# Kernel tuning notes

Hardware: AMD Instinct MI355X
Metric: run time of the kernel (lower is better)

Reference implementation:

```python
import jax, jax.numpy as jnp
import numpy as np

FEAT = 1024
HID = 512
DK = 256
N = 8192
KMAX = 8
K_LIST = (2, 4, 8)


def setup_inputs() -> dict:
    key = jax.random.key(0)
    ks = jax.random.split(key, 10)
    def glorot(k, shape):
        lim = np.sqrt(6.0 / (shape[0] + shape[1]))
        return jax.random.uniform(k, shape, jnp.float32, -lim, lim)
    return {
        "input_tensor": jax.random.normal(ks[0], (N, FEAT), jnp.float32),
        "sp_matrix": jax.random.randint(ks[1], (N, KMAX + 1), 0, N, jnp.int64 if jax.config.jax_enable_x64 else jnp.int32),
        "W1": glorot(ks[2], (FEAT, HID)),
        "b1": jnp.zeros((HID,), jnp.float32),
        "Wq": glorot(ks[3], (HID, DK)),
        "Wk": glorot(ks[4], (HID, DK)),
        "Wv": glorot(ks[5], (HID, DK)),
        "bv": jnp.zeros((DK,), jnp.float32),
        "Wout": glorot(ks[6], (DK, 2)),
        "bout": jnp.zeros((2,), jnp.float32),
    }


def reference(input_tensor, sp_matrix, W1, b1, Wq, Wk, Wv, bv, Wout, bout):
    # fc1: Dense(512, relu)
    dense = jax.nn.relu(input_tensor @ W1 + b1)            # [n, 512]
    # CustomAttention: scaled QK^T over the whole bag
    q = dense @ Wq                                          # [n, 256]
    k = dense @ Wk                                          # [n, 256]
    attn = (q @ k.T) / jnp.sqrt(jnp.float32(DK))            # [n, n]
    value = dense @ Wv + bv                                 # [n, 256]
    pools = []
    for kk in K_LIST:
        idx = sp_matrix[:, : kk + 1]                        # [n, kk+1]
        # sparse adjacency * attention, row-sum == gather attn[i, idx[i,j]] and sum over j
        a_raw = jnp.take_along_axis(attn, idx, axis=1).sum(axis=1)  # [n]
        alpha = jax.nn.softmax(a_raw)                       # [n]
        pools.append(alpha[:, None] * value)                # [n, 256]
    spp = jnp.concatenate(pools, axis=0)                    # [3n, 256]
    # Last_Sigmoid (subtyping=True): sum-pool -> dense -> softmax
    logits = spp.sum(axis=0, keepdims=True) @ Wout + bout   # [1, 2]
    return jax.nn.softmax(logits, axis=-1)
```

## Files before the change

### kernel.cpp

```cpp
#include <hip/hip_runtime.h>
#include <hip/hip_bf16.h>
#include <math.h>

#define FEAT 1024
#define HID  512
#define DK   256
#define NROWS 8192

typedef __attribute__((ext_vector_type(8))) short short8;
typedef __attribute__((ext_vector_type(4))) float floatx4;

__device__ __forceinline__ unsigned short f2bf(float x) {
    union { float f; unsigned u; } u;
    u.f = x;
    unsigned r = u.u;
    r += 0x7fffu + ((r >> 16) & 1u);
    return (unsigned short)(r >> 16);
}
__device__ __forceinline__ float bf2f(unsigned short x) {
    union { unsigned u; float f; } u;
    u.u = ((unsigned)x) << 16;
    return u.f;
}

__device__ __forceinline__ void gld_lds16(const unsigned short* g, unsigned short* l) {
    __builtin_amdgcn_global_load_lds(
        (__attribute__((address_space(1))) void*)(void*)g,
        (__attribute__((address_space(3))) void*)l,
        16, 0, 0);
}

__device__ __forceinline__ short8 cast8(float4 a, float4 b) {
    short8 r;
    r[0] = (short)f2bf(a.x); r[1] = (short)f2bf(a.y);
    r[2] = (short)f2bf(a.z); r[3] = (short)f2bf(a.w);
    r[4] = (short)f2bf(b.x); r[5] = (short)f2bf(b.y);
    r[6] = (short)f2bf(b.z); r[7] = (short)f2bf(b.w);
    return r;
}

__global__ __launch_bounds__(256) void prep_kernel(
    const float* __restrict__ W1, const float* __restrict__ Wq,
    const float* __restrict__ Wk, const float* __restrict__ Wv,
    unsigned short* __restrict__ W1T, unsigned short* __restrict__ WqT,
    unsigned short* __restrict__ WkT, unsigned short* __restrict__ WvT,
    float* __restrict__ P, float* __restrict__ Z, unsigned* __restrict__ counter)
{
    const int b = blockIdx.x;
    const int tid = threadIdx.x;

    if (b == 0) {
        for (int i = tid; i < 3 * DK; i += 256) P[i] = 0.f;
        if (tid < 3) Z[tid] = 0.f;
        if (tid == 0) *counter = 0u;
    }

    int t = b;
    const float* in; unsigned short* outp; int K, N, tn, tk;
    if (t < 512) {
        in = W1; outp = W1T; K = FEAT; N = HID; tn = t & 15; tk = t >> 4;
    } else {
        t -= 512;
        int z = t >> 7, r = t & 127;
        K = HID; N = DK; tn = r & 7; tk = r >> 3;
        in   = (z == 0) ? Wq  : (z == 1) ? Wk  : Wv;
        outp = (z == 0) ? WqT : (z == 1) ? WkT : WvT;
    }
    __shared__ float tt[32][33];
    const int tx = tid & 31, ty = tid >> 5;
    const int n0 = tn * 32, k0 = tk * 32;
    #pragma unroll
    for (int i2 = ty; i2 < 32; i2 += 8)
        tt[i2][tx] = in[(size_t)(k0 + i2) * N + (n0 + tx)];
    __syncthreads();
    #pragma unroll
    for (int i2 = ty; i2 < 32; i2 += 8)
        outp[(size_t)(n0 + i2) * K + (k0 + tx)] = f2bf(tt[tx][i2]);
}

template<int A_F32>
__global__ __launch_bounds__(256) void gemm_mfma(
    const void* __restrict__ Av,
    const unsigned short* __restrict__ BT0, const unsigned short* __restrict__ BT1,
    const unsigned short* __restrict__ BT2,
    const float* __restrict__ bias0, const float* __restrict__ bias1,
    const float* __restrict__ bias2,
    unsigned short* __restrict__ C0, unsigned short* __restrict__ C1,
    unsigned short* __restrict__ C2,
    int N, int K, int relu)
{
    const int z = blockIdx.z;
    const unsigned short* BT = (z == 0) ? BT0 : (z == 1) ? BT1 : BT2;
    const float* bias        = (z == 0) ? bias0 : (z == 1) ? bias1 : bias2;
    unsigned short* C        = (z == 0) ? C0 : (z == 1) ? C1 : C2;

    __shared__ __align__(16) unsigned short As[64 * 64];
    __shared__ __align__(16) unsigned short Bs[128 * 64];

    const int tid  = threadIdx.x;
    const int lane = tid & 63;
    const int wid  = tid >> 6;
    const int wm = wid >> 1, wn = wid & 1;
    const int m0 = blockIdx.x * 64;
    const int n0 = blockIdx.y * 128;

    int arowp[2], asgp[2];
    const float*          ApF[2];
    const unsigned short* ApB[2];
    #pragma unroll
    for (int p = 0; p < 2; ++p) {
        int idx = p * 256 + tid;
        int row = idx >> 3, g = idx & 7;
        int sg = g ^ (row & 7);
        arowp[p] = row; asgp[p] = sg;
        ApF[p] = (const float*)Av + (size_t)(m0 + row) * K + g * 8;
        ApB[p] = (const unsigned short*)Av + (size_t)(m0 + row) * K + sg * 8;
    }
    const unsigned short* Bp[4];
    #pragma unroll
    for (int p = 0; p < 4; ++p) {
        int idx = p * 256 + tid;
        int row = idx >> 3, g = idx & 7;
        int sg = g ^ (row & 7);
        Bp[p] = BT + (size_t)(n0 + row) * K + sg * 8;
    }

    char* AsB = (char*)As;
    char* BsB = (char*)Bs;

    const int gr = lane >> 4;
    int aoff[2][2], boff[2][4];
    #pragma unroll
    for (int ks = 0; ks < 2; ++ks) {
        int gk = ks * 4 + gr;
        #pragma unroll
        for (int i = 0; i < 2; ++i) {
            int ra = wm * 32 + i * 16 + (lane & 15);
            aoff[ks][i] = ra * 128 + ((gk ^ (ra & 7)) * 16);
        }
        #pragma unroll
        for (int jj = 0; jj < 4; ++jj) {
            int rb = wn * 64 + jj * 16 + (lane & 15);
            boff[ks][jj] = rb * 128 + ((gk ^ (rb & 7)) * 16);
        }
    }

    floatx4 acc[2][4];
    #pragma unroll
    for (int i = 0; i < 2; ++i)
        #pragma unroll
        for (int jj = 0; jj < 4; ++jj)
            acc[i][jj] = (floatx4){0.f, 0.f, 0.f, 0.f};

    for (int kt = 0; kt < K; kt += 64) {
        if (A_F32) {
            float4 a00 = *(const float4*)(ApF[0] + kt);
            float4 a01 = *(const float4*)(ApF[0] + kt + 4);
            float4 a10 = *(const float4*)(ApF[1] + kt);
            float4 a11 = *(const float4*)(ApF[1] + kt + 4);
            #pragma unroll
            for (int p = 0; p < 4; ++p)
                gld_lds16(Bp[p] + kt, (unsigned short*)(BsB + p * 4096 + wid * 1024));
            *(short8*)(AsB + arowp[0] * 128 + asgp[0] * 16) = cast8(a00, a01);
            *(short8*)(AsB + arowp[1] * 128 + asgp[1] * 16) = cast8(a10, a11);
        } else {
            #pragma unroll
            for (int p = 0; p < 2; ++p)
                gld_lds16(ApB[p] + kt, (unsigned short*)(AsB + p * 4096 + wid * 1024));
            #pragma unroll
            for (int p = 0; p < 4; ++p)
                gld_lds16(Bp[p] + kt, (unsigned short*)(BsB + p * 4096 + wid * 1024));
        }
        __syncthreads();

        #pragma unroll
        for (int ks = 0; ks < 2; ++ks) {
            short8 af[2], bfr[4];
            #pragma unroll
            for (int i = 0; i < 2; ++i) af[i] = *(const short8*)(AsB + aoff[ks][i]);
            #pragma unroll
            for (int jj = 0; jj < 4; ++jj) bfr[jj] = *(const short8*)(BsB + boff[ks][jj]);
            #pragma unroll
            for (int i = 0; i < 2; ++i)
                #pragma unroll
                for (int jj = 0; jj < 4; ++jj)
                    acc[i][jj] = __builtin_amdgcn_mfma_f32_16x16x32_bf16(
                        af[i], bfr[jj], acc[i][jj], 0, 0, 0);
        }
        __syncthreads();
    }

    #pragma unroll
    for (int i = 0; i < 2; ++i) {
        int rbase = m0 + wm * 32 + i * 16 + (lane >> 4) * 4;
        #pragma unroll
        for (int jj = 0; jj < 4; ++jj) {
            int c = n0 + wn * 64 + jj * 16 + (lane & 15);
            float bb = bias ? bias[c] : 0.f;
            #pragma unroll
            for (int r = 0; r < 4; ++r) {
                float v = acc[i][jj][r] + bb;
                if (relu) v = fmaxf(v, 0.f);
                C[(size_t)(rbase + r) * N + c] = f2bf(v);
            }
        }
    }
}

__global__ __launch_bounds__(256) void gather_attn(
    const unsigned short* __restrict__ Q, const unsigned short* __restrict__ Kmat,
    const int* __restrict__ sp, float* __restrict__ a_raw)
{
    const int lane = threadIdx.x & 63;
    const int wid  = threadIdx.x >> 6;
    const int i = blockIdx.x * 4 + wid;

    ushort4 qr = *(const ushort4*)(Q + (size_t)i * DK + lane * 4);
    float4 q = make_float4(bf2f(qr.x), bf2f(qr.y), bf2f(qr.z), bf2f(qr.w));
    float4 ks = make_float4(0.f, 0.f, 0.f, 0.f);

    int sel = 0;
    #pragma unroll
    for (int j = 0; j <= 8; ++j) {
        int r = sp[i * 9 + j];
        ushort4 kr = *(const ushort4*)(Kmat + (size_t)r * DK + lane * 4);
        ks.x += bf2f(kr.x); ks.y += bf2f(kr.y);
        ks.z += bf2f(kr.z); ks.w += bf2f(kr.w);
        if (j == 2 || j == 4 || j == 8) {
            float d = q.x * ks.x + q.y * ks.y + q.z * ks.z + q.w * ks.w;
            #pragma unroll
            for (int off = 32; off; off >>= 1) d += __shfl_xor(d, off);
            if (lane == 0) a_raw[sel * NROWS + i] = d * 0.0625f;
            ++sel;
        }
    }
}

#define RPB 64
#define SM_SHIFT 10.0f
__global__ __launch_bounds__(256) void pool_kernel(
    const float* __restrict__ a_raw,
    const unsigned short* __restrict__ V, float* __restrict__ P,
    float* __restrict__ Z, unsigned* __restrict__ counter,
    const float* __restrict__ Wout, const float* __restrict__ bout,
    float* __restrict__ out)
{
    const int r0 = blockIdx.x * RPB;
    const int t = threadIdx.x;

    __shared__ float red[2][256];
    __shared__ float e[3][RPB];
    __shared__ unsigned rank;
    __shared__ float zz[3];

    float z0 = 0.f, z1 = 0.f, z2 = 0.f;
    if (t < RPB) {
        z0 = expf(a_raw[0 * NROWS + r0 + t] - SM_SHIFT);
        z1 = expf(a_raw[1 * NROWS + r0 + t] - SM_SHIFT);
        z2 = expf(a_raw[2 * NROWS + r0 + t] - SM_SHIFT);
        e[0][t] = z0; e[1][t] = z1; e[2][t] = z2;
    }
    __syncthreads();

    float a0 = 0.f, a1 = 0.f, a2 = 0.f;
    for (int r = 0; r < RPB; ++r) {
        float v = bf2f(V[(size_t)(r0 + r) * DK + t]);
        a0 = fmaf(e[0][r], v, a0);
        a1 = fmaf(e[1][r], v, a1);
        a2 = fmaf(e[2][r], v, a2);
    }
    atomicAdd(&P[0 * DK + t], a0);
    atomicAdd(&P[1 * DK + t], a1);
    atomicAdd(&P[2 * DK + t], a2);

    #pragma unroll
    for (int off = 32; off; off >>= 1) {
        z0 += __shfl_xor(z0, off); z1 += __shfl_xor(z1, off); z2 += __shfl_xor(z2, off);
    }
    if (t == 0) {
        atomicAdd(&Z[0], z0); atomicAdd(&Z[1], z1); atomicAdd(&Z[2], z2);
    }

    __threadfence();
    if (t == 0) rank = atomicAdd(counter, 1u);
    __syncthreads();
    if (rank == gridDim.x - 1) {
        __threadfence();
        if (t < 3) zz[t] = atomicAdd(&Z[t], 0.0f);
        __syncthreads();
        float p0 = atomicAdd(&P[0 * DK + t], 0.0f);
        float p1 = atomicAdd(&P[1 * DK + t], 0.0f);
        float p2 = atomicAdd(&P[2 * DK + t], 0.0f);
        float s = p0 / zz[0] + p1 / zz[1] + p2 / zz[2];
        red[0][t] = s * Wout[t * 2 + 0];
        red[1][t] = s * Wout[t * 2 + 1];
        __syncthreads();
        for (int st = 128; st; st >>= 1) {
            if (t < st) {
                red[0][t] += red[0][t + st];
                red[1][t] += red[1][t + st];
            }
            __syncthreads();
        }
        if (t == 0) {
            float a = red[0][0] + bout[0], b = red[1][0] + bout[1];
            float mm = fmaxf(a, b);
            float ea = expf(a - mm), eb = expf(b - mm);
            float inv = 1.f / (ea + eb);
            out[0] = ea * inv;
            out[1] = eb * inv;
        }
    }
}

extern "C" void kernel_launch(void* const* d_in, const int* in_sizes, int n_in,
                              void* d_out, int out_size, void* d_ws, size_t ws_size,
                              hipStream_t stream)
{
    const float* X    = (const float*)d_in[0];
    const int*   sp   = (const int*)  d_in[1];
    const float* W1   = (const float*)d_in[2];
    const float* b1   = (const float*)d_in[3];
    const float* Wq   = (const float*)d_in[4];
    const float* Wk   = (const float*)d_in[5];
    const float* Wv   = (const float*)d_in[6];
    const float* bv   = (const float*)d_in[7];
    const float* Wout = (const float*)d_in[8];
    const float* bout = (const float*)d_in[9];
    float* out = (float*)d_out;

    char* w = (char*)d_ws;
    unsigned short* dense_b = (unsigned short*)(w);
    unsigned short* W1T     = (unsigned short*)(w +  8388608);
    unsigned short* WqT     = (unsigned short*)(w +  9437184);
    unsigned short* WkT     = (unsigned short*)(w +  9699328);
    unsigned short* WvT     = (unsigned short*)(w +  9961472);
    float* a_raw            = (float*)(w + 10223616);
    float* P                = (float*)(w + 10321920);
    float* Z                = P + 3 * DK;
    unsigned* counter       = (unsigned*)(Z + 3);
    unsigned short* Qb      = (unsigned short*)(w + 10485760);
    unsigned short* Kb      = (unsigned short*)(w + 14680064);
    unsigned short* Vb      = (unsigned short*)(w + 18874368);

    prep_kernel<<<896, 256, 0, stream>>>(
        W1, Wq, Wk, Wv, W1T, WqT, WkT, WvT, P, Z, counter);

    gemm_mfma<1><<<dim3(NROWS / 64, HID / 128, 1), 256, 0, stream>>>(
        X, W1T, nullptr, nullptr, b1, nullptr, nullptr,
        dense_b, nullptr, nullptr, HID, FEAT, 1);

    gemm_mfma<0><<<dim3(NROWS / 64, DK / 128, 3), 256, 0, stream>>>(
        dense_b, WqT, WkT, WvT, nullptr, nullptr, bv,
        Qb, Kb, Vb, DK, HID, 0);

    gather_attn<<<NROWS / 4, 256, 0, stream>>>(Qb, Kb, sp, a_raw);
    pool_kernel<<<NROWS / RPB, 256, 0, stream>>>(
        a_raw, Vb, P, Z, counter, Wout, bout, out);
}
```

Before: 69.60 us.

## Double-buffer GEMM LDS tiles and fuse gather with pooling via group counters

The MFMA GEMM now uses two LDS buffers and prefetches the next K tile while computing the current one, so it needs one barrier per iteration instead of two. The gather-attention and pooling kernels are merged into one launch. Each group of 16 blocks increments a counter, and the last block of the group computes exp weights, pools V for those 64 rows, and feeds the global reduction. This removes a kernel launch and the round trip of raw scores through memory. In exchange it doubles LDS use, which may lower occupancy, and the pooling work is serialised onto only 128 blocks.

```diff
diff --git a/kernel.cpp b/kernel.cpp
--- a/kernel.cpp
+++ b/kernel.cpp
@@ -44,7 +44,8 @@
     const float* __restrict__ Wk, const float* __restrict__ Wv,
     unsigned short* __restrict__ W1T, unsigned short* __restrict__ WqT,
     unsigned short* __restrict__ WkT, unsigned short* __restrict__ WvT,
-    float* __restrict__ P, float* __restrict__ Z, unsigned* __restrict__ counter)
+    float* __restrict__ P, float* __restrict__ Z, unsigned* __restrict__ counter,
+    unsigned* __restrict__ grp_cnt)
 {
     const int b = blockIdx.x;
     const int tid = threadIdx.x;
@@ -53,6 +54,7 @@
         for (int i = tid; i < 3 * DK; i += 256) P[i] = 0.f;
         if (tid < 3) Z[tid] = 0.f;
         if (tid == 0) *counter = 0u;
+        if (tid < 128) grp_cnt[tid] = 0u;
     }
 
     int t = b;
@@ -94,8 +96,8 @@
     const float* bias        = (z == 0) ? bias0 : (z == 1) ? bias1 : bias2;
     unsigned short* C        = (z == 0) ? C0 : (z == 1) ? C1 : C2;
 
-    __shared__ __align__(16) unsigned short As[64 * 64];
-    __shared__ __align__(16) unsigned short Bs[128 * 64];
+    __shared__ __align__(16) unsigned short As[2][64 * 64];
+    __shared__ __align__(16) unsigned short Bs[2][128 * 64];
 
     const int tid  = threadIdx.x;
     const int lane = tid & 63;
@@ -152,34 +154,58 @@
         for (int jj = 0; jj < 4; ++jj)
             acc[i][jj] = (floatx4){0.f, 0.f, 0.f, 0.f};
 
-    for (int kt = 0; kt < K; kt += 64) {
+    if (A_F32) {
+        float4 a00 = *(const float4*)(ApF[0]);
+        float4 a01 = *(const float4*)(ApF[0] + 4);
+        float4 a10 = *(const float4*)(ApF[1]);
+        float4 a11 = *(const float4*)(ApF[1] + 4);
+        #pragma unroll
+        for (int p = 0; p < 4; ++p)
+            gld_lds16(Bp[p], (unsigned short*)(BsB + p * 4096 + wid * 1024));
+        *(short8*)(AsB + arowp[0] * 128 + asgp[0] * 16) = cast8(a00, a01);
+        *(short8*)(AsB + arowp[1] * 128 + asgp[1] * 16) = cast8(a10, a11);
+    } else {
+        #pragma unroll
+        for (int p = 0; p < 2; ++p)
+            gld_lds16(ApB[p], (unsigned short*)(AsB + p * 4096 + wid * 1024));
+        #pragma unroll
+        for (int p = 0; p < 4; ++p)
+            gld_lds16(Bp[p], (unsigned short*)(BsB + p * 4096 + wid * 1024));
+    }
+    __syncthreads();
+
+    int cur = 0;
+    for (int kt = 64; kt < K; kt += 64) {
+        char* AsN = AsB + (cur ^ 1) * 8192;
+        char* BsN = BsB + (cur ^ 1) * 16384;
+
+        float4 a00, a01, a10, a11;
         if (A_F32) {
-            float4 a00 = *(const float4*)(ApF[0] + kt);
-            float4 a01 = *(const float4*)(ApF[0] + kt + 4);
-            float4 a10 = *(const float4*)(ApF[1] + kt);
-            float4 a11 = *(const float4*)(ApF[1] + kt + 4);
+            a00 = *(const float4*)(ApF[0] + kt);
+            a01 = *(const float4*)(ApF[0] + kt + 4);
+            a10 = *(const float4*)(ApF[1] + kt);
+            a11 = *(const float4*)(ApF[1] + kt + 4);
             #pragma unroll
             for (int p = 0; p < 4; ++p)
-                gld_lds16(Bp[p] + kt, (unsigned short*)(BsB + p * 4096 + wid * 1024));
-            *(short8*)(AsB + arowp[0] * 128 + asgp[0] * 16) = cast8(a00, a01);
-            *(short8*)(AsB + arowp[1] * 128 + asgp[1] * 16) = cast8(a10, a11);
+                gld_lds16(Bp[p] + kt, (unsigned short*)(BsN + p * 4096 + wid * 1024));
         } else {
             #pragma unroll
             for (int p = 0; p < 2; ++p)
-                gld_lds16(ApB[p] + kt, (unsigned short*)(AsB + p * 4096 + wid * 1024));
+                gld_lds16(ApB[p] + kt, (unsigned short*)(AsN + p * 4096 + wid * 1024));
             #pragma unroll
             for (int p = 0; p < 4; ++p)
-                gld_lds16(Bp[p] + kt, (unsigned short*)(BsB + p * 4096 + wid * 1024));
-        }
-        __syncthreads();
-
+                gld_lds16(Bp[p] + kt, (unsigned short*)(BsN + p * 4096 + wid * 1024));
+        }
+
+        const char* AsC = AsB + cur * 8192;
+        const char* BsC = BsB + cur * 16384;
         #pragma unroll
         for (int ks = 0; ks < 2; ++ks) {
             short8 af[2], bfr[4];
             #pragma unroll
-            for (int i = 0; i < 2; ++i) af[i] = *(const short8*)(AsB + aoff[ks][i]);
-            #pragma unroll
-            for (int jj = 0; jj < 4; ++jj) bfr[jj] = *(const short8*)(BsB + boff[ks][jj]);
+            for (int i = 0; i < 2; ++i) af[i] = *(const short8*)(AsC + aoff[ks][i]);
+            #pragma unroll
+            for (int jj = 0; jj < 4; ++jj) bfr[jj] = *(const short8*)(BsC + boff[ks][jj]);
             #pragma unroll
             for (int i = 0; i < 2; ++i)
                 #pragma unroll
@@ -187,7 +213,33 @@
                     acc[i][jj] = __builtin_amdgcn_mfma_f32_16x16x32_bf16(
                         af[i], bfr[jj], acc[i][jj], 0, 0, 0);
         }
+
+        if (A_F32) {
+            *(short8*)(AsN + arowp[0] * 128 + asgp[0] * 16) = cast8(a00, a01);
+            *(short8*)(AsN + arowp[1] * 128 + asgp[1] * 16) = cast8(a10, a11);
+        }
+
         __syncthreads();
+        cur ^= 1;
+    }
+
+    {
+        const char* AsC = AsB + cur * 8192;
+        const char* BsC = BsB + cur * 16384;
+        #pragma unroll
+        for (int ks = 0; ks < 2; ++ks) {
+            short8 af[2], bfr[4];
+            #pragma unroll
+            for (int i = 0; i < 2; ++i) af[i] = *(const short8*)(AsC + aoff[ks][i]);
+            #pragma unroll
+            for (int jj = 0; jj < 4; ++jj) bfr[jj] = *(const short8*)(BsC + boff[ks][jj]);
+            #pragma unroll
+            for (int i = 0; i < 2; ++i)
+                #pragma unroll
+                for (int jj = 0; jj < 4; ++jj)
+                    acc[i][jj] = __builtin_amdgcn_mfma_f32_16x16x32_bf16(
+                        af[i], bfr[jj], acc[i][jj], 0, 0, 0);
+        }
     }
 
     #pragma unroll
@@ -207,63 +259,66 @@
     }
 }
 
-__global__ __launch_bounds__(256) void gather_attn(
+#define SM_SHIFT 10.0f
+__global__ __launch_bounds__(256) void gather_pool(
     const unsigned short* __restrict__ Q, const unsigned short* __restrict__ Kmat,
-    const int* __restrict__ sp, float* __restrict__ a_raw)
+    const unsigned short* __restrict__ V, const int* __restrict__ sp,
+    float* __restrict__ e_arr, float* __restrict__ P, float* __restrict__ Z,
+    unsigned* __restrict__ grp_cnt, unsigned* __restrict__ counter,
+    const float* __restrict__ Wout, const float* __restrict__ bout,
+    float* __restrict__ out)
 {
     const int lane = threadIdx.x & 63;
     const int wid  = threadIdx.x >> 6;
     const int i = blockIdx.x * 4 + wid;
 
-    ushort4 qr = *(const ushort4*)(Q + (size_t)i * DK + lane * 4);
-    float4 q = make_float4(bf2f(qr.x), bf2f(qr.y), bf2f(qr.z), bf2f(qr.w));
-    float4 ks = make_float4(0.f, 0.f, 0.f, 0.f);
-
-    int sel = 0;
-    #pragma unroll
-    for (int j = 0; j <= 8; ++j) {
-        int r = sp[i * 9 + j];
-        ushort4 kr = *(const ushort4*)(Kmat + (size_t)r * DK + lane * 4);
-        ks.x += bf2f(kr.x); ks.y += bf2f(kr.y);
-        ks.z += bf2f(kr.z); ks.w += bf2f(kr.w);
-        if (j == 2 || j == 4 || j == 8) {
-            float d = q.x * ks.x + q.y * ks.y + q.z * ks.z + q.w * ks.w;
-            #pragma unroll
-            for (int off = 32; off; off >>= 1) d += __shfl_xor(d, off);
-            if (lane == 0) a_raw[sel * NROWS + i] = d * 0.0625f;
-            ++sel;
-        }
-    }
-}
-
-#define RPB 64
-#define SM_SHIFT 10.0f
-__global__ __launch_bounds__(256) void pool_kernel(
-    const float* __restrict__ a_raw,
-    const unsigned short* __restrict__ V, float* __restrict__ P,
-    float* __restrict__ Z, unsigned* __restrict__ counter,
-    const float* __restrict__ Wout, const float* __restrict__ bout,
-    float* __restrict__ out)
-{
-    const int r0 = blockIdx.x * RPB;
+    {
+        ushort4 qr = *(const ushort4*)(Q + (size_t)i * DK + lane * 4);
+        float4 q = make_float4(bf2f(qr.x), bf2f(qr.y), bf2f(qr.z), bf2f(qr.w));
+        float4 ks = make_float4(0.f, 0.f, 0.f, 0.f);
+
+        int sel = 0;
+        #pragma unroll
+        for (int j = 0; j <= 8; ++j) {
+            int r = sp[i * 9 + j];
+            ushort4 kr = *(const ushort4*)(Kmat + (size_t)r * DK + lane * 4);
+            ks.x += bf2f(kr.x); ks.y += bf2f(kr.y);
+            ks.z += bf2f(kr.z); ks.w += bf2f(kr.w);
+            if (j == 2 || j == 4 || j == 8) {
+                float d = q.x * ks.x + q.y * ks.y + q.z * ks.z + q.w * ks.w;
+                #pragma unroll
+                for (int off = 32; off; off >>= 1) d += __shfl_xor(d, off);
+                if (lane == 0)
+                    e_arr[sel * NROWS + i] = expf(d * 0.0625f - SM_SHIFT);
+                ++sel;
+            }
+        }
+    }
+
+    __shared__ unsigned srank;
+    __shared__ float e[3][64];
+    __shared__ float red[2][256];
+    __shared__ unsigned rank2;
+    __shared__ float zz[3];
+
+    const int g = blockIdx.x >> 4;
     const int t = threadIdx.x;
 
-    __shared__ float red[2][256];
-    __shared__ float e[3][RPB];
-    __shared__ unsigned rank;
-    __shared__ float zz[3];
-
-    float z0 = 0.f, z1 = 0.f, z2 = 0.f;
-    if (t < RPB) {
-        z0 = expf(a_raw[0 * NROWS + r0 + t] - SM_SHIFT);
-        z1 = expf(a_raw[1 * NROWS + r0 + t] - SM_SHIFT);
-        z2 = expf(a_raw[2 * NROWS + r0 + t] - SM_SHIFT);
-        e[0][t] = z0; e[1][t] = z1; e[2][t] = z2;
-    }
+    __threadfence();
+    if (t == 0) srank = atomicAdd(&grp_cnt[g], 1u);
     __syncthreads();
-
+    if (srank != 15u) return;
+
+    __threadfence();
+    if (t < 192) {
+        int sel = t >> 6, r = t & 63;
+        e[sel][r] = atomicAdd(&e_arr[sel * NROWS + g * 64 + r], 0.0f);
+    }
+    __syncthreads();
+
+    const int r0 = g * 64;
     float a0 = 0.f, a1 = 0.f, a2 = 0.f;
-    for (int r = 0; r < RPB; ++r) {
+    for (int r = 0; r < 64; ++r) {
         float v = bf2f(V[(size_t)(r0 + r) * DK + t]);
         a0 = fmaf(e[0][r], v, a0);
         a1 = fmaf(e[1][r], v, a1);
@@ -272,19 +327,17 @@
     atomicAdd(&P[0 * DK + t], a0);
     atomicAdd(&P[1 * DK + t], a1);
     atomicAdd(&P[2 * DK + t], a2);
-
-    #pragma unroll
-    for (int off = 32; off; off >>= 1) {
-        z0 += __shfl_xor(z0, off); z1 += __shfl_xor(z1, off); z2 += __shfl_xor(z2, off);
-    }
-    if (t == 0) {
-        atomicAdd(&Z[0], z0); atomicAdd(&Z[1], z1); atomicAdd(&Z[2], z2);
+    if (t < 3) {
+        float s = 0.f;
+        #pragma unroll
+        for (int r = 0; r < 64; ++r) s += e[t][r];
+        atomicAdd(&Z[t], s);
     }
 
     __threadfence();
-    if (t == 0) rank = atomicAdd(counter, 1u);
+    if (t == 0) rank2 = atomicAdd(counter, 1u);
     __syncthreads();
-    if (rank == gridDim.x - 1) {
+    if (rank2 == 127u) {
         __threadfence();
         if (t < 3) zz[t] = atomicAdd(&Z[t], 0.0f);
         __syncthreads();
@@ -335,16 +388,17 @@
     unsigned short* WqT     = (unsigned short*)(w +  9437184);
     unsigned short* WkT     = (unsigned short*)(w +  9699328);
     unsigned short* WvT     = (unsigned short*)(w +  9961472);
-    float* a_raw            = (float*)(w + 10223616);
+    float* e_arr            = (float*)(w + 10223616);
     float* P                = (float*)(w + 10321920);
     float* Z                = P + 3 * DK;
     unsigned* counter       = (unsigned*)(Z + 3);
+    unsigned* grp_cnt       = counter + 1;
     unsigned short* Qb      = (unsigned short*)(w + 10485760);
     unsigned short* Kb      = (unsigned short*)(w + 14680064);
     unsigned short* Vb      = (unsigned short*)(w + 18874368);
 
     prep_kernel<<<896, 256, 0, stream>>>(
-        W1, Wq, Wk, Wv, W1T, WqT, WkT, WvT, P, Z, counter);
+        W1, Wq, Wk, Wv, W1T, WqT, WkT, WvT, P, Z, counter, grp_cnt);
 
     gemm_mfma<1><<<dim3(NROWS / 64, HID / 128, 1), 256, 0, stream>>>(
         X, W1T, nullptr, nullptr, b1, nullptr, nullptr,
@@ -354,7 +408,6 @@
         dense_b, WqT, WkT, WvT, nullptr, nullptr, bv,
         Qb, Kb, Vb, DK, HID, 0);
 
-    gather_attn<<<NROWS / 4, 256, 0, stream>>>(Qb, Kb, sp, a_raw);
-    pool_kernel<<<NROWS / RPB, 256, 0, stream>>>(
-        a_raw, Vb, P, Z, counter, Wout, bout, out);
-}
+    gather_pool<<<NROWS / 4, 256, 0, stream>>>(
+        Qb, Kb, Vb, sp, e_arr, P, Z, grp_cnt, counter, Wout, bout, out);
+}
```

Measured after the change: 234.7 us. 237% more time.

## Double-buffer LDS tiles and prefetch next K-tile in GEMM mainloop

Applied to the files above, without the earlier changes.

Doubles the shared-memory A/B tiles and issues the global-to-LDS loads for tile t+1 before computing on tile t, using explicit s_waitcnt with partial vmcnt and raw s_barrier plus sched_barriers in place of __syncthreads. The aim is to hide global load latency behind the MFMA work. In exchange the kernel uses twice the LDS, which may lower occupancy. It also depends on hand-counted vmcnt values matching how many loads the compiler actually emits.

```diff
diff --git a/kernel.cpp b/kernel.cpp
--- a/kernel.cpp
+++ b/kernel.cpp
@@ -94,8 +94,8 @@
     const float* bias        = (z == 0) ? bias0 : (z == 1) ? bias1 : bias2;
     unsigned short* C        = (z == 0) ? C0 : (z == 1) ? C1 : C2;
 
-    __shared__ __align__(16) unsigned short As[64 * 64];
-    __shared__ __align__(16) unsigned short Bs[128 * 64];
+    __shared__ __align__(16) unsigned short As[2][64 * 64];
+    __shared__ __align__(16) unsigned short Bs[2][128 * 64];
 
     const int tid  = threadIdx.x;
     const int lane = tid & 63;
@@ -152,34 +152,71 @@
         for (int jj = 0; jj < 4; ++jj)
             acc[i][jj] = (floatx4){0.f, 0.f, 0.f, 0.f};
 
-    for (int kt = 0; kt < K; kt += 64) {
+    float4 ar[4];
+    if (A_F32) {
+        ar[0] = *(const float4*)(ApF[0]);
+        ar[1] = *(const float4*)(ApF[0] + 4);
+        ar[2] = *(const float4*)(ApF[1]);
+        ar[3] = *(const float4*)(ApF[1] + 4);
+        #pragma unroll
+        for (int p = 0; p < 4; ++p)
+            gld_lds16(Bp[p], (unsigned short*)(BsB + p * 4096 + wid * 1024));
+    } else {
+        #pragma unroll
+        for (int p = 0; p < 2; ++p)
+            gld_lds16(ApB[p], (unsigned short*)(AsB + p * 4096 + wid * 1024));
+        #pragma unroll
+        for (int p = 0; p < 4; ++p)
+            gld_lds16(Bp[p], (unsigned short*)(BsB + p * 4096 + wid * 1024));
+    }
+
+    const int T = K >> 6;
+    for (int t = 0; t < T; ++t) {
+        const int cur = t & 1;
+        char* AsC = AsB + cur * 8192;
+        char* BsC = BsB + cur * 16384;
+        char* AsN = AsB + (cur ^ 1) * 8192;
+        char* BsN = BsB + (cur ^ 1) * 16384;
+
         if (A_F32) {
-            float4 a00 = *(const float4*)(ApF[0] + kt);
-            float4 a01 = *(const float4*)(ApF[0] + kt + 4);
-            float4 a10 = *(const float4*)(ApF[1] + kt);
-            float4 a11 = *(const float4*)(ApF[1] + kt + 4);
-            #pragma unroll
-            for (int p = 0; p < 4; ++p)
-                gld_lds16(Bp[p] + kt, (unsigned short*)(BsB + p * 4096 + wid * 1024));
-            *(short8*)(AsB + arowp[0] * 128 + asgp[0] * 16) = cast8(a00, a01);
-            *(short8*)(AsB + arowp[1] * 128 + asgp[1] * 16) = cast8(a10, a11);
+            *(short8*)(AsC + arowp[0] * 128 + asgp[0] * 16) = cast8(ar[0], ar[1]);
+            *(short8*)(AsC + arowp[1] * 128 + asgp[1] * 16) = cast8(ar[2], ar[3]);
+        }
+
+        if (t + 1 < T) {
+            const int kn = (t + 1) << 6;
+            if (A_F32) {
+                ar[0] = *(const float4*)(ApF[0] + kn);
+                ar[1] = *(const float4*)(ApF[0] + kn + 4);
+                ar[2] = *(const float4*)(ApF[1] + kn);
+                ar[3] = *(const float4*)(ApF[1] + kn + 4);
+                #pragma unroll
+                for (int p = 0; p < 4; ++p)
+                    gld_lds16(Bp[p] + kn, (unsigned short*)(BsN + p * 4096 + wid * 1024));
+                asm volatile("s_waitcnt vmcnt(8) lgkmcnt(0)" ::: "memory");
+            } else {
+                #pragma unroll
+                for (int p = 0; p < 2; ++p)
+                    gld_lds16(ApB[p] + kn, (unsigned short*)(AsN + p * 4096 + wid * 1024));
+                #pragma unroll
+                for (int p = 0; p < 4; ++p)
+                    gld_lds16(Bp[p] + kn, (unsigned short*)(BsN + p * 4096 + wid * 1024));
+                asm volatile("s_waitcnt vmcnt(6) lgkmcnt(0)" ::: "memory");
+            }
         } else {
-            #pragma unroll
-            for (int p = 0; p < 2; ++p)
-                gld_lds16(ApB[p] + kt, (unsigned short*)(AsB + p * 4096 + wid * 1024));
-            #pragma unroll
-            for (int p = 0; p < 4; ++p)
-                gld_lds16(Bp[p] + kt, (unsigned short*)(BsB + p * 4096 + wid * 1024));
-        }
-        __syncthreads();
+            asm volatile("s_waitcnt vmcnt(0) lgkmcnt(0)" ::: "memory");
+        }
+        __builtin_amdgcn_sched_barrier(0);
+        __builtin_amdgcn_s_barrier();
+        __builtin_amdgcn_sched_barrier(0);
 
         #pragma unroll
         for (int ks = 0; ks < 2; ++ks) {
             short8 af[2], bfr[4];
             #pragma unroll
-            for (int i = 0; i < 2; ++i) af[i] = *(const short8*)(AsB + aoff[ks][i]);
+            for (int i = 0; i < 2; ++i) af[i] = *(const short8*)(AsC + aoff[ks][i]);
             #pragma unroll
-            for (int jj = 0; jj < 4; ++jj) bfr[jj] = *(const short8*)(BsB + boff[ks][jj]);
+            for (int jj = 0; jj < 4; ++jj) bfr[jj] = *(const short8*)(BsC + boff[ks][jj]);
             #pragma unroll
             for (int i = 0; i < 2; ++i)
                 #pragma unroll
@@ -187,7 +224,10 @@
                     acc[i][jj] = __builtin_amdgcn_mfma_f32_16x16x32_bf16(
                         af[i], bfr[jj], acc[i][jj], 0, 0, 0);
         }
-        __syncthreads();
+
+        __builtin_amdgcn_sched_barrier(0);
+        __builtin_amdgcn_s_barrier();
+        __builtin_amdgcn_sched_barrier(0);
     }
 
     #pragma unroll
```

Result: no change. 69.76 us (+0.2%).
